# Kernel tuning notes

Measured on AMD Instinct MI355X. Metric: run time of the kernel, lower is better.

Reference implementation:

```python
import jax, jax.numpy as jnp
import numpy as np

HIDDEN_DIM = 256
CLIP_LEN = 2
B, NQ, T, D = 64, 10, 2048, 256


def setup_inputs() -> dict:
    key = jax.random.key(0)
    ks = jax.random.split(key, 10)
    s = 1.0 / np.sqrt(HIDDEN_DIM)  # torch GRU/Linear init scale
    return {
        "pred_logits": jax.random.normal(ks[0], (B, NQ, 2), jnp.float32),
        "pred_spans": jax.random.uniform(ks[1], (B, NQ, 2), jnp.float32),
        "memory": jax.random.normal(ks[2], (B, T, D), jnp.float32),
        "src_vid": jax.random.normal(ks[3], (B, T, D), jnp.float32),
        "W_ih": jax.random.normal(ks[4], (3 * D, D), jnp.float32) * s,
        "W_hh": jax.random.normal(ks[5], (3 * D, D), jnp.float32) * s,
        "b_ih": jax.random.normal(ks[6], (3 * D,), jnp.float32) * s,
        "b_hh": jax.random.normal(ks[7], (3 * D,), jnp.float32) * s,
        "W_sal": jax.random.normal(ks[8], (D, D), jnp.float32) * s,
        "b_sal": jax.random.normal(ks[9], (D,), jnp.float32) * s,
    }


def _gru_last_hidden(x, W_ih, W_hh, b_ih, b_hh):
    # x: [B, T, D] -> final hidden state [B, D] (torch nn.GRU, h0 = 0)
    b, t, d = x.shape
    gi = jnp.einsum("btd,gd->btg", x, W_ih) + b_ih  # [B, T, 3D], precompute input gates

    def step(h, gi_t):
        gh = jnp.einsum("bd,gd->bg", h, W_hh) + b_hh
        ir, iz, inn = jnp.split(gi_t, 3, axis=-1)
        hr, hz, hn = jnp.split(gh, 3, axis=-1)
        r = jax.nn.sigmoid(ir + hr)
        z = jax.nn.sigmoid(iz + hz)
        n = jnp.tanh(inn + r * hn)
        h_new = (1.0 - z) * n + z * h
        return h_new, None

    h0 = jnp.zeros((b, d), x.dtype)
    hT, _ = jax.lax.scan(step, h0, jnp.swapaxes(gi, 0, 1))
    return hT


def reference(pred_logits, pred_spans, memory, src_vid, W_ih, W_hh, b_ih, b_hh, W_sal, b_sal):
    b, t, d = memory.shape
    # top-1 span selection (sort descending, take first == argmax of class-0 prob)
    scores = jax.nn.softmax(pred_logits, axis=-1)[..., 0]  # [B, NQ]
    best = jnp.argmax(scores, axis=-1)  # [B]
    span = jnp.take_along_axis(pred_spans, best[:, None, None], axis=1)[:, 0, :]  # [B, 2] (cx, w)
    cx, w = span[:, 0], span[:, 1]
    xx = jnp.stack([cx - 0.5 * w, cx + 0.5 * w], axis=-1) * (t * CLIP_LEN)
    se = jnp.floor(xx / CLIP_LEN).astype(jnp.int32)  # [B, 2] start/end frame indices
    start = jnp.clip(se[:, 0], 0, t - 1)
    end_eff = jnp.minimum(se[:, 1], t - 1)
    # on-device dynamic slice + zero pad to fixed length T (replaces python loop)
    idx = start[:, None] + jnp.arange(t)[None, :]  # [B, T]
    valid = idx <= end_eff[:, None]  # empty slice if end < start
    idx_c = jnp.clip(idx, 0, t - 1)
    sliced = jnp.take_along_axis(src_vid, idx_c[..., None], axis=1) * valid[..., None].astype(src_vid.dtype)
    # GRU over padded slice, take last hidden
    hidden = _gru_last_hidden(sliced, W_ih, W_hh, b_ih, b_hh)  # [B, D]
    weight = jnp.einsum("bd,btd->bt", hidden, src_vid)  # [B, T]
    mem = memory * weight[..., None] + memory
    proj = jnp.einsum("btd,ed->bte", mem, W_sal) + b_sal
    saliency = jnp.sum(proj, axis=-1) / np.sqrt(HIDDEN_DIM)
    return saliency  # [B, T]
```

## Files before the change

kernel.cpp:

```cpp
#include <hip/hip_runtime.h>
#include <hip/hip_bf16.h>
#include <stdint.h>

#define T_SEQ 2048
#define DDIM 256
#define G3 768
#define NB 64
#define NQR 10

typedef _Float16 h2f __attribute__((ext_vector_type(2)));
typedef unsigned u32x4 __attribute__((ext_vector_type(4)));

__device__ __forceinline__ float fdot2u(unsigned a, unsigned b, float c) {
    return __builtin_amdgcn_fdot2(__builtin_bit_cast(h2f, a),
                                  __builtin_bit_cast(h2f, b), c, false);
}
__device__ __forceinline__ unsigned packf16(float a, float b) {
    auto p = __builtin_amdgcn_cvt_pkrtz(a, b);
    return __builtin_bit_cast(unsigned, p);
}
__device__ __forceinline__ float unpk(unsigned u, int hi) {
    unsigned w = hi ? (u >> 16) : u;
    h2f p = __builtin_bit_cast(h2f, w);
    return (float)p[0];
}
__device__ __forceinline__ float sigmf(float x) { return 1.0f / (1.0f + __expf(-x)); }
__device__ __forceinline__ float tanhff(float x) {
    float ax = fabsf(x);
    float e = __expf(2.0f * ax);
    float t = 1.0f - 2.0f / (e + 1.0f);
    return copysignf(t, x);
}

#define PIN4(x) asm volatile("" : "+v"(x))

__global__ __launch_bounds__(256) void k_prologue(
    const float* __restrict__ logits, const float* __restrict__ spans,
    const float* __restrict__ W_sal, const float* __restrict__ b_sal,
    int* __restrict__ meta, float* __restrict__ wcol, float* __restrict__ bsum) {
    int tid = threadIdx.x;
    if (tid < NB) {
        int b = tid;
        float bestv = -1e30f; int best = 0;
        for (int q = 0; q < NQR; ++q) {
            float l0 = logits[(b * NQR + q) * 2 + 0];
            float l1 = logits[(b * NQR + q) * 2 + 1];
            float sc = sigmf(l0 - l1);
            if (sc > bestv) { bestv = sc; best = q; }
        }
        float cx = spans[(b * NQR + best) * 2 + 0];
        float w  = spans[(b * NQR + best) * 2 + 1];
        float x0 = (cx - 0.5f * w) * (float)(T_SEQ * 2);
        float x1 = (cx + 0.5f * w) * (float)(T_SEQ * 2);
        int se0 = (int)floorf(x0 * 0.5f);
        int se1 = (int)floorf(x1 * 0.5f);
        int start = min(max(se0, 0), T_SEQ - 1);
        int end_eff = min(se1, T_SEQ - 1);
        int len = end_eff - start + 1;
        if (len < 0) len = 0;
        meta[b] = start; meta[NB + b] = len;
    }
    float acc = 0.f;
    for (int e = 0; e < DDIM; ++e) acc += W_sal[e * DDIM + tid];
    wcol[tid] = acc;
    if (tid < 64) {
        float p = b_sal[tid] + b_sal[tid + 64] + b_sal[tid + 128] + b_sal[tid + 192];
        for (int off = 32; off; off >>= 1) p += __shfl_down(p, off, 64);
        if (tid == 0) *bsum = p;
    }
}

__global__ __launch_bounds__(256) void k_prep(
    const float* __restrict__ W_ih, const float* __restrict__ W_hh,
    float* __restrict__ wt_ih, unsigned* __restrict__ w4) {
    int g = blockIdx.x, k = threadIdx.x;
    wt_ih[k * G3 + g] = W_ih[g * DDIM + k];
    if (k < 128) {
        unsigned v = packf16(W_hh[g * DDIM + 2 * k], W_hh[g * DDIM + 2 * k + 1]);
        w4[((k >> 2) * G3 + g) * 4 + (k & 3)] = v;
    }
}

__global__ __launch_bounds__(256) void k_gemm(
    const float* __restrict__ src_vid, const float* __restrict__ wt_ih,
    const float* __restrict__ b_ih, const int* __restrict__ meta,
    unsigned* __restrict__ gi2, int t0, int tc, int TC) {
    int b = blockIdx.y;
    int len = meta[NB + b];
    int tb = t0 + blockIdx.x * 16;
    int tcap = t0 + tc; if (tcap > len) tcap = len;
    if (tb >= tcap) return;
    int start = meta[b];
    int j = threadIdx.x;
    int nval = tcap - tb; if (nval > 16) nval = 16;
    float aR[16], aZ[16], aN[16];
    float bR = b_ih[j], bZ = b_ih[DDIM + j], bN = b_ih[2 * DDIM + j];
#pragma unroll
    for (int r = 0; r < 16; ++r) { aR[r] = bR; aZ[r] = bZ; aN[r] = bN; }
    const float* xb = src_vid + ((size_t)b * T_SEQ + start + tb) * DDIM;
    for (int kq = 0; kq < 64; ++kq) {
        float4 xq[16];
#pragma unroll
        for (int r = 0; r < 16; ++r) {
            if (r < nval) xq[r] = *(const float4*)(xb + r * DDIM + kq * 4);
            else          xq[r] = make_float4(0.f, 0.f, 0.f, 0.f);
        }
#pragma unroll
        for (int e = 0; e < 4; ++e) {
            int k = kq * 4 + e;
            float wR = wt_ih[k * G3 + j];
            float wZ = wt_ih[k * G3 + DDIM + j];
            float wN = wt_ih[k * G3 + 2 * DDIM + j];
#pragma unroll
            for (int r = 0; r < 16; ++r) {
                float xv = (e == 0) ? xq[r].x : (e == 1) ? xq[r].y : (e == 2) ? xq[r].z : xq[r].w;
                aR[r] = fmaf(xv, wR, aR[r]);
                aZ[r] = fmaf(xv, wZ, aZ[r]);
                aN[r] = fmaf(xv, wN, aN[r]);
            }
        }
    }
    unsigned* go = gi2 + ((size_t)b * TC + (tb - t0)) * 384;
    for (int r = 0; r < nval; ++r) {
        float oR = __shfl_xor(aR[r], 1, 64);
        float oZ = __shfl_xor(aZ[r], 1, 64);
        float oN = __shfl_xor(aN[r], 1, 64);
        if (!(j & 1)) {
            unsigned* gw = go + (size_t)r * 384 + (j >> 1);
            gw[0]   = packf16(aR[r], oR);
            gw[128] = packf16(aZ[r], oZ);
            gw[256] = packf16(aN[r], oN);
        }
    }
}

__global__ void __launch_bounds__(512)
__attribute__((amdgpu_waves_per_eu(2, 2))) k_gru(
    const unsigned* __restrict__ gi2, const unsigned* __restrict__ w4,
    const float* __restrict__ b_ih, const float* __restrict__ b_hh,
    const int* __restrict__ meta, float* __restrict__ h_state,
    int t0, int t1, int TC) {
    int b = blockIdx.x, tid = threadIdx.x;
    int c = tid & 255, half = tid >> 8;
    int len = meta[NB + b];

    u32x4 wrq[16], wzq[16], wnq[16];
    const u32x4* w4v = (const u32x4*)w4;
    const u32x4* wb = w4v + (size_t)(half * 16) * G3;
#pragma unroll
    for (int q = 0; q < 16; ++q) {
        wrq[q] = wb[q * G3 + c];
        wzq[q] = wb[q * G3 + 256 + c];
        wnq[q] = wb[q * G3 + 512 + c];
    }
#pragma unroll
    for (int q = 0; q < 16; ++q) { PIN4(wrq[q]); PIN4(wzq[q]); PIN4(wnq[q]); }

    float bhR = (half == 0) ? b_hh[c] : 0.f;
    float bhZ = (half == 0) ? b_hh[256 + c] : 0.f;
    float bhN = (half == 0) ? b_hh[512 + c] : 0.f;
    float biR = b_ih[c], biZ = b_ih[256 + c], biN = b_ih[512 + c];

    __shared__ unsigned hl[128];
    __shared__ float pl[3][256];

    float h = 0.f;
    if (half == 0) {
        if (t0 != 0) h = h_state[b * DDIM + c];
        float hp = __shfl_xor(h, 1, 64);
        if (!(c & 1)) hl[c >> 1] = packf16(h, hp);
    }

    const unsigned* gb2 = gi2 + (size_t)b * TC * 384 + (c >> 1);
    int sel = c & 1;
    float gR = biR, gZ = biZ, gN = biN;
    if (half == 0 && t0 < t1 && t0 < len) {
        gR = unpk(gb2[0], sel); gZ = unpk(gb2[128], sel); gN = unpk(gb2[256], sel);
    }
    __syncthreads();

    for (int t = t0; t < t1; ++t) {
        float nR = biR, nZ = biZ, nN = biN;
        int tn = t + 1;
        if (half == 0 && tn < t1 && tn < len) {
            const unsigned* gp = gb2 + (size_t)(tn - t0) * 384;
            nR = unpk(gp[0], sel); nZ = unpk(gp[128], sel); nN = unpk(gp[256], sel);
        }
#pragma unroll
        for (int q = 0; q < 16; ++q) { PIN4(wrq[q]); PIN4(wzq[q]); PIN4(wnq[q]); }
        float r0 = bhR, z0 = bhZ, n0 = bhN, r1 = 0.f, z1 = 0.f, n1 = 0.f;
        const u32x4* hb = (const u32x4*)hl + half * 16;
#pragma unroll
        for (int q = 0; q < 16; ++q) {
            u32x4 h4 = hb[q];
            r0 = fdot2u(h4.x, wrq[q].x, r0);
            z0 = fdot2u(h4.x, wzq[q].x, z0);
            n0 = fdot2u(h4.x, wnq[q].x, n0);
            r1 = fdot2u(h4.y, wrq[q].y, r1);
            z1 = fdot2u(h4.y, wzq[q].y, z1);
            n1 = fdot2u(h4.y, wnq[q].y, n1);
            r0 = fdot2u(h4.z, wrq[q].z, r0);
            z0 = fdot2u(h4.z, wzq[q].z, z0);
            n0 = fdot2u(h4.z, wnq[q].z, n0);
            r1 = fdot2u(h4.w, wrq[q].w, r1);
            z1 = fdot2u(h4.w, wzq[q].w, z1);
            n1 = fdot2u(h4.w, wnq[q].w, n1);
        }
        float hr = r0 + r1, hz = z0 + z1, hn = n0 + n1;
        if (half == 1) {
            pl[0][c] = hr; pl[1][c] = hz; pl[2][c] = hn;
        }
        __syncthreads();
        if (half == 0) {
            hr += pl[0][c]; hz += pl[1][c]; hn += pl[2][c];
            float r = sigmf(gR + hr);
            float z = sigmf(gZ + hz);
            float n = tanhff(gN + r * hn);
            h = (1.0f - z) * n + z * h;
            float hp = __shfl_xor(h, 1, 64);
            if (!(c & 1)) hl[c >> 1] = packf16(h, hp);
        }
        gR = nR; gZ = nZ; gN = nN;
        __syncthreads();
    }
    if (half == 0) h_state[b * DDIM + c] = h;
}

__global__ __launch_bounds__(256) void k_epi(
    const float* __restrict__ memory, const float* __restrict__ src_vid,
    const float* __restrict__ h_state, const float* __restrict__ wcol,
    const float* __restrict__ bsum, float* __restrict__ out) {
    int wid = blockIdx.x * 4 + (threadIdx.x >> 6);
    int lane = threadIdx.x & 63;
    int b = wid >> 11;
    int t = wid & 2047;
    const float4* mp = (const float4*)(memory + ((size_t)b * T_SEQ + t) * DDIM);
    const float4* sp = (const float4*)(src_vid + ((size_t)b * T_SEQ + t) * DDIM);
    const float4* hp = (const float4*)(h_state + b * DDIM);
    const float4* wp = (const float4*)wcol;
    float4 m = mp[lane], s = sp[lane], hv = hp[lane], wc = wp[lane];
    float s1 = m.x * wc.x + m.y * wc.y + m.z * wc.z + m.w * wc.w;
    float s2 = hv.x * s.x + hv.y * s.y + hv.z * s.z + hv.w * s.w;
    for (int off = 32; off; off >>= 1) {
        s1 += __shfl_down(s1, off, 64);
        s2 += __shfl_down(s2, off, 64);
    }
    if (lane == 0) out[(size_t)b * T_SEQ + t] = ((1.0f + s2) * s1 + *bsum) * 0.0625f;
}

extern "C" void kernel_launch(void* const* d_in, const int* in_sizes, int n_in,
                              void* d_out, int out_size, void* d_ws, size_t ws_size,
                              hipStream_t stream) {
    const float* logits  = (const float*)d_in[0];
    const float* spans   = (const float*)d_in[1];
    const float* memory  = (const float*)d_in[2];
    const float* src_vid = (const float*)d_in[3];
    const float* W_ih    = (const float*)d_in[4];
    const float* W_hh    = (const float*)d_in[5];
    const float* b_ih    = (const float*)d_in[6];
    const float* b_hh    = (const float*)d_in[7];
    const float* W_sal   = (const float*)d_in[8];
    const float* b_sal   = (const float*)d_in[9];
    float* out = (float*)d_out;
    char* ws = (char*)d_ws;

    const size_t OFF_META = 0;
    const size_t OFF_WCOL = 1024;
    const size_t OFF_BSUM = 2048;
    const size_t OFF_H    = 4096;
    const size_t OFF_W4   = 69632;
    const size_t OFF_WTIH = 462848;
    const size_t OFF_GI   = 1249280;

    int* meta       = (int*)(ws + OFF_META);
    float* wcol     = (float*)(ws + OFF_WCOL);
    float* bsum     = (float*)(ws + OFF_BSUM);
    float* h_state  = (float*)(ws + OFF_H);
    unsigned* w4    = (unsigned*)(ws + OFF_W4);
    float* wt_ih    = (float*)(ws + OFF_WTIH);
    unsigned* gi2   = (unsigned*)(ws + OFF_GI);

    size_t gi_cap = (ws_size > OFF_GI) ? (ws_size - OFF_GI) : 0;
    long long tc_max = (long long)(gi_cap / ((size_t)NB * 384 * 4));
    int TC = (tc_max > T_SEQ) ? T_SEQ : (int)tc_max;
    if (TC < 16) TC = 16;

    k_prologue<<<dim3(1), dim3(256), 0, stream>>>(logits, spans, W_sal, b_sal, meta, wcol, bsum);
    k_prep<<<dim3(G3), dim3(256), 0, stream>>>(W_ih, W_hh, wt_ih, w4);
    for (int t0 = 0; t0 < T_SEQ; t0 += TC) {
        int tc = T_SEQ - t0; if (tc > TC) tc = TC;
        k_gemm<<<dim3((tc + 15) / 16, NB), dim3(256), 0, stream>>>(
            src_vid, wt_ih, b_ih, meta, gi2, t0, tc, TC);
        k_gru<<<dim3(NB), dim3(512), 0, stream>>>(
            gi2, w4, b_ih, b_hh, meta, h_state, t0, t0 + tc, TC);
    }
    k_epi<<<dim3(NB * T_SEQ / 4), dim3(256), 0, stream>>>(
        memory, src_vid, h_state, wcol, bsum, out);
}
```

Before: 2.993 ms.

## Compute GRU r/z recurrent gates with MFMA waves, n gate on separate waves

Splits the per-batch GRU block into 8 waves that compute the r and z recurrent matvecs with 16x16x32 f16 MFMA, using W_hh fragments pre-swizzled by a new prep kernel, plus 4 waves that compute the n-gate dot products with fdot2 and run the gate update. The aim is to shorten the per-step latency of the serial recurrence by offloading two thirds of the recurrent work to matrix units and running it alongside the n-gate work. Each MFMA uses the broadcast hidden vector as the A operand, so only one of its 16 rows is used. The change also adds an extra weight layout in the workspace, which shrinks the gi chunk capacity, and keeps two barriers per step.

```diff
diff --git a/kernel.cpp b/kernel.cpp
--- a/kernel.cpp
+++ b/kernel.cpp
@@ -9,6 +9,8 @@
 #define NQR 10
 
 typedef _Float16 h2f __attribute__((ext_vector_type(2)));
+typedef _Float16 f16x8 __attribute__((ext_vector_type(8)));
+typedef float f32x4 __attribute__((ext_vector_type(4)));
 typedef unsigned u32x4 __attribute__((ext_vector_type(4)));
 
 __device__ __forceinline__ float fdot2u(unsigned a, unsigned b, float c) {
@@ -20,9 +22,8 @@
     return __builtin_bit_cast(unsigned, p);
 }
 __device__ __forceinline__ float unpk(unsigned u, int hi) {
-    unsigned w = hi ? (u >> 16) : u;
-    h2f p = __builtin_bit_cast(h2f, w);
-    return (float)p[0];
+    h2f p = __builtin_bit_cast(h2f, u);
+    return hi ? (float)p[1] : (float)p[0];
 }
 __device__ __forceinline__ float sigmf(float x) { return 1.0f / (1.0f + __expf(-x)); }
 __device__ __forceinline__ float tanhff(float x) {
@@ -31,8 +32,6 @@
     float t = 1.0f - 2.0f / (e + 1.0f);
     return copysignf(t, x);
 }
-
-#define PIN4(x) asm volatile("" : "+v"(x))
 
 __global__ __launch_bounds__(256) void k_prologue(
     const float* __restrict__ logits, const float* __restrict__ spans,
@@ -79,6 +78,18 @@
         unsigned v = packf16(W_hh[g * DDIM + 2 * k], W_hh[g * DDIM + 2 * k + 1]);
         w4[((k >> 2) * G3 + g) * 4 + (k & 3)] = v;
     }
+}
+
+__global__ __launch_bounds__(256) void k_prep2(
+    const float* __restrict__ W_hh, unsigned* __restrict__ wfrag) {
+    int u = blockIdx.x * 256 + threadIdx.x;
+    int jj = u & 3;
+    int l  = (u >> 2) & 63;
+    int kc = (u >> 8) & 7;
+    int wt = u >> 11;
+    int col = wt * 16 + (l & 15);
+    int k = kc * 32 + ((l >> 4) << 3) + jj * 2;
+    wfrag[u] = packf16(W_hh[col * DDIM + k], W_hh[col * DDIM + k + 1]);
 }
 
 __global__ __launch_bounds__(256) void k_gemm(
@@ -134,96 +145,112 @@
     }
 }
 
-__global__ void __launch_bounds__(512)
-__attribute__((amdgpu_waves_per_eu(2, 2))) k_gru(
+__global__ void __launch_bounds__(768) k_gru(
     const unsigned* __restrict__ gi2, const unsigned* __restrict__ w4,
+    const unsigned* __restrict__ wfrag,
     const float* __restrict__ b_ih, const float* __restrict__ b_hh,
     const int* __restrict__ meta, float* __restrict__ h_state,
     int t0, int t1, int TC) {
     int b = blockIdx.x, tid = threadIdx.x;
-    int c = tid & 255, half = tid >> 8;
+    int lane = tid & 63, w = tid >> 6;
     int len = meta[NB + b];
 
-    u32x4 wrq[16], wzq[16], wnq[16];
-    const u32x4* w4v = (const u32x4*)w4;
-    const u32x4* wb = w4v + (size_t)(half * 16) * G3;
-#pragma unroll
-    for (int q = 0; q < 16; ++q) {
-        wrq[q] = wb[q * G3 + c];
-        wzq[q] = wb[q * G3 + 256 + c];
-        wnq[q] = wb[q * G3 + 512 + c];
-    }
-#pragma unroll
-    for (int q = 0; q < 16; ++q) { PIN4(wrq[q]); PIN4(wzq[q]); PIN4(wnq[q]); }
-
-    float bhR = (half == 0) ? b_hh[c] : 0.f;
-    float bhZ = (half == 0) ? b_hh[256 + c] : 0.f;
-    float bhN = (half == 0) ? b_hh[512 + c] : 0.f;
-    float biR = b_ih[c], biZ = b_ih[256 + c], biN = b_ih[512 + c];
-
     __shared__ unsigned hl[128];
-    __shared__ float pl[3][256];
-
-    float h = 0.f;
-    if (half == 0) {
+    __shared__ float rz[512];
+
+    const f32x4 zf = {0.f, 0.f, 0.f, 0.f};
+
+    if (w < 8) {
+        int g = w >> 2;
+        int tq = w & 3;
+        u32x4 bf[32];
+        const u32x4* wfr = (const u32x4*)wfrag;
+#pragma unroll
+        for (int t4 = 0; t4 < 4; ++t4)
+#pragma unroll
+            for (int kc = 0; kc < 8; ++kc) {
+                int wt = g * 16 + tq * 4 + t4;
+                bf[t4 * 8 + kc] = wfr[(size_t)(wt * 8 + kc) * 64 + lane];
+            }
+        __syncthreads();
+        for (int t = t0; t < t1; ++t) {
+            f32x4 cf[4];
+            const u32x4* hb = (const u32x4*)hl;
+#pragma unroll
+            for (int kc = 0; kc < 8; ++kc) {
+                u32x4 av = hb[kc * 4 + (lane >> 4)];
+                f16x8 af = __builtin_bit_cast(f16x8, av);
+#pragma unroll
+                for (int t4 = 0; t4 < 4; ++t4) {
+                    cf[t4] = __builtin_amdgcn_mfma_f32_16x16x32_f16(
+                        af, __builtin_bit_cast(f16x8, bf[t4 * 8 + kc]),
+                        (kc == 0) ? zf : cf[t4], 0, 0, 0);
+                }
+            }
+            if (lane < 16) {
+#pragma unroll
+                for (int t4 = 0; t4 < 4; ++t4)
+                    rz[g * 256 + (tq * 4 + t4) * 16 + lane] = cf[t4][0];
+            }
+            __syncthreads();
+            __syncthreads();
+        }
+    } else {
+        int c = tid - 512;
+        u32x4 nq[32];
+        const u32x4* w4v = (const u32x4*)w4;
+#pragma unroll
+        for (int q = 0; q < 32; ++q) nq[q] = w4v[(size_t)q * G3 + 512 + c];
+
+        float bhR = b_hh[c], bhZ = b_hh[256 + c], bhN = b_hh[512 + c];
+        float biR = b_ih[c], biZ = b_ih[256 + c], biN = b_ih[512 + c];
+
+        float h = 0.f;
         if (t0 != 0) h = h_state[b * DDIM + c];
-        float hp = __shfl_xor(h, 1, 64);
-        if (!(c & 1)) hl[c >> 1] = packf16(h, hp);
-    }
-
-    const unsigned* gb2 = gi2 + (size_t)b * TC * 384 + (c >> 1);
-    int sel = c & 1;
-    float gR = biR, gZ = biZ, gN = biN;
-    if (half == 0 && t0 < t1 && t0 < len) {
-        gR = unpk(gb2[0], sel); gZ = unpk(gb2[128], sel); gN = unpk(gb2[256], sel);
-    }
-    __syncthreads();
-
-    for (int t = t0; t < t1; ++t) {
-        float nR = biR, nZ = biZ, nN = biN;
-        int tn = t + 1;
-        if (half == 0 && tn < t1 && tn < len) {
-            const unsigned* gp = gb2 + (size_t)(tn - t0) * 384;
-            nR = unpk(gp[0], sel); nZ = unpk(gp[128], sel); nN = unpk(gp[256], sel);
-        }
-#pragma unroll
-        for (int q = 0; q < 16; ++q) { PIN4(wrq[q]); PIN4(wzq[q]); PIN4(wnq[q]); }
-        float r0 = bhR, z0 = bhZ, n0 = bhN, r1 = 0.f, z1 = 0.f, n1 = 0.f;
-        const u32x4* hb = (const u32x4*)hl + half * 16;
-#pragma unroll
-        for (int q = 0; q < 16; ++q) {
-            u32x4 h4 = hb[q];
-            r0 = fdot2u(h4.x, wrq[q].x, r0);
-            z0 = fdot2u(h4.x, wzq[q].x, z0);
-            n0 = fdot2u(h4.x, wnq[q].x, n0);
-            r1 = fdot2u(h4.y, wrq[q].y, r1);
-            z1 = fdot2u(h4.y, wzq[q].y, z1);
-            n1 = fdot2u(h4.y, wnq[q].y, n1);
-            r0 = fdot2u(h4.z, wrq[q].z, r0);
-            z0 = fdot2u(h4.z, wzq[q].z, z0);
-            n0 = fdot2u(h4.z, wnq[q].z, n0);
-            r1 = fdot2u(h4.w, wrq[q].w, r1);
-            z1 = fdot2u(h4.w, wzq[q].w, z1);
-            n1 = fdot2u(h4.w, wnq[q].w, n1);
-        }
-        float hr = r0 + r1, hz = z0 + z1, hn = n0 + n1;
-        if (half == 1) {
-            pl[0][c] = hr; pl[1][c] = hz; pl[2][c] = hn;
+        {
+            float hp = __shfl_xor(h, 1, 64);
+            if (!(c & 1)) hl[c >> 1] = packf16(h, hp);
+        }
+        const unsigned* gb2 = gi2 + (size_t)b * TC * 384 + (c >> 1);
+        int sel = c & 1;
+        float gR = biR, gZ = biZ, gN = biN;
+        if (t0 < t1 && t0 < len) {
+            gR = unpk(gb2[0], sel); gZ = unpk(gb2[128], sel); gN = unpk(gb2[256], sel);
         }
         __syncthreads();
-        if (half == 0) {
-            hr += pl[0][c]; hz += pl[1][c]; hn += pl[2][c];
+
+        for (int t = t0; t < t1; ++t) {
+            float nR = biR, nZ = biZ, nN = biN;
+            int tn = t + 1;
+            if (tn < t1 && tn < len) {
+                const unsigned* gp = gb2 + (size_t)(tn - t0) * 384;
+                nR = unpk(gp[0], sel); nZ = unpk(gp[128], sel); nN = unpk(gp[256], sel);
+            }
+            float a0 = 0.f, a1 = 0.f, a2 = 0.f, a3 = 0.f;
+            const u32x4* hb = (const u32x4*)hl;
+#pragma unroll
+            for (int q = 0; q < 32; ++q) {
+                u32x4 h4 = hb[q];
+                a0 = fdot2u(h4.x, nq[q].x, a0);
+                a1 = fdot2u(h4.y, nq[q].y, a1);
+                a2 = fdot2u(h4.z, nq[q].z, a2);
+                a3 = fdot2u(h4.w, nq[q].w, a3);
+            }
+            float hn = bhN + (a0 + a1) + (a2 + a3);
+            __syncthreads();
+            float hr = rz[c] + bhR;
+            float hz = rz[256 + c] + bhZ;
             float r = sigmf(gR + hr);
             float z = sigmf(gZ + hz);
             float n = tanhff(gN + r * hn);
             h = (1.0f - z) * n + z * h;
             float hp = __shfl_xor(h, 1, 64);
             if (!(c & 1)) hl[c >> 1] = packf16(h, hp);
-        }
-        gR = nR; gZ = nZ; gN = nN;
-        __syncthreads();
-    }
-    if (half == 0) h_state[b * DDIM + c] = h;
+            gR = nR; gZ = nZ; gN = nN;
+            __syncthreads();
+        }
+        h_state[b * DDIM + c] = h;
+    }
 }
 
 __global__ __launch_bounds__(256) void k_epi(
@@ -269,14 +296,16 @@
     const size_t OFF_BSUM = 2048;
     const size_t OFF_H    = 4096;
     const size_t OFF_W4   = 69632;
-    const size_t OFF_WTIH = 462848;
-    const size_t OFF_GI   = 1249280;
+    const size_t OFF_FRAG = 462848;
+    const size_t OFF_WTIH = 856064;
+    const size_t OFF_GI   = 1642496;
 
     int* meta       = (int*)(ws + OFF_META);
     float* wcol     = (float*)(ws + OFF_WCOL);
     float* bsum     = (float*)(ws + OFF_BSUM);
     float* h_state  = (float*)(ws + OFF_H);
     unsigned* w4    = (unsigned*)(ws + OFF_W4);
+    unsigned* wfrag = (unsigned*)(ws + OFF_FRAG);
     float* wt_ih    = (float*)(ws + OFF_WTIH);
     unsigned* gi2   = (unsigned*)(ws + OFF_GI);
 
@@ -287,12 +316,13 @@
 
     k_prologue<<<dim3(1), dim3(256), 0, stream>>>(logits, spans, W_sal, b_sal, meta, wcol, bsum);
     k_prep<<<dim3(G3), dim3(256), 0, stream>>>(W_ih, W_hh, wt_ih, w4);
+    k_prep2<<<dim3(384), dim3(256), 0, stream>>>(W_hh, wfrag);
     for (int t0 = 0; t0 < T_SEQ; t0 += TC) {
         int tc = T_SEQ - t0; if (tc > TC) tc = TC;
         k_gemm<<<dim3((tc + 15) / 16, NB), dim3(256), 0, stream>>>(
             src_vid, wt_ih, b_ih, meta, gi2, t0, tc, TC);
-        k_gru<<<dim3(NB), dim3(512), 0, stream>>>(
-            gi2, w4, b_ih, b_hh, meta, h_state, t0, t0 + tc, TC);
+        k_gru<<<dim3(NB), dim3(768), 0, stream>>>(
+            gi2, w4, wfrag, b_ih, b_hh, meta, h_state, t0, t0 + tc, TC);
     }
     k_epi<<<dim3(NB * T_SEQ / 4), dim3(256), 0, stream>>>(
         memory, src_vid, h_state, wcol, bsum, out);
```

Measured after the change: 3.224 ms. 1.08x slower.

## Restructure GRU step to reduce K within wavefronts and double-buffer hidden state

Applied to the files above, without the earlier changes.

The recurrent GRU kernel is reorganized so each wavefront owns 32 output columns and splits the K dimension across four 16-lane groups, reducing partial sums with cross-lane shuffles instead of a shared-memory exchange between two thread halves. The hidden state is double-buffered in LDS, which removes one of the two block barriers per timestep. The LDS layout of h is permuted so each lane group reads its own K slice. This trades the second barrier and LDS round trip for extra shuffle instructions and drops the register-pinning asm and waves-per-eu hint, which may change register allocation.

```diff
diff --git a/kernel.cpp b/kernel.cpp
--- a/kernel.cpp
+++ b/kernel.cpp
@@ -20,9 +20,8 @@
     return __builtin_bit_cast(unsigned, p);
 }
 __device__ __forceinline__ float unpk(unsigned u, int hi) {
-    unsigned w = hi ? (u >> 16) : u;
-    h2f p = __builtin_bit_cast(h2f, w);
-    return (float)p[0];
+    h2f p = __builtin_bit_cast(h2f, u);
+    return hi ? (float)p[1] : (float)p[0];
 }
 __device__ __forceinline__ float sigmf(float x) { return 1.0f / (1.0f + __expf(-x)); }
 __device__ __forceinline__ float tanhff(float x) {
@@ -31,8 +30,6 @@
     float t = 1.0f - 2.0f / (e + 1.0f);
     return copysignf(t, x);
 }
-
-#define PIN4(x) asm volatile("" : "+v"(x))
 
 __global__ __launch_bounds__(256) void k_prologue(
     const float* __restrict__ logits, const float* __restrict__ spans,
@@ -134,96 +131,105 @@
     }
 }
 
-__global__ void __launch_bounds__(512)
-__attribute__((amdgpu_waves_per_eu(2, 2))) k_gru(
+__global__ void __launch_bounds__(512) k_gru(
     const unsigned* __restrict__ gi2, const unsigned* __restrict__ w4,
     const float* __restrict__ b_ih, const float* __restrict__ b_hh,
     const int* __restrict__ meta, float* __restrict__ h_state,
     int t0, int t1, int TC) {
     int b = blockIdx.x, tid = threadIdx.x;
-    int c = tid & 255, half = tid >> 8;
+    int lane = tid & 63, w = tid >> 6;
+    int kq = lane >> 4, lc = lane & 15;
+    int c0 = w * 32 + lc * 2;
     int len = meta[NB + b];
 
-    u32x4 wrq[16], wzq[16], wnq[16];
+    u32x4 wq[8][3][2];
     const u32x4* w4v = (const u32x4*)w4;
-    const u32x4* wb = w4v + (size_t)(half * 16) * G3;
-#pragma unroll
-    for (int q = 0; q < 16; ++q) {
-        wrq[q] = wb[q * G3 + c];
-        wzq[q] = wb[q * G3 + 256 + c];
-        wnq[q] = wb[q * G3 + 512 + c];
-    }
-#pragma unroll
-    for (int q = 0; q < 16; ++q) { PIN4(wrq[q]); PIN4(wzq[q]); PIN4(wnq[q]); }
-
-    float bhR = (half == 0) ? b_hh[c] : 0.f;
-    float bhZ = (half == 0) ? b_hh[256 + c] : 0.f;
-    float bhN = (half == 0) ? b_hh[512 + c] : 0.f;
-    float biR = b_ih[c], biZ = b_ih[256 + c], biN = b_ih[512 + c];
-
-    __shared__ unsigned hl[128];
-    __shared__ float pl[3][256];
+#pragma unroll
+    for (int q = 0; q < 8; ++q)
+#pragma unroll
+        for (int ga = 0; ga < 3; ++ga)
+#pragma unroll
+            for (int cc = 0; cc < 2; ++cc)
+                wq[q][ga][cc] = w4v[(size_t)(kq * 8 + q) * G3 + ga * 256 + c0 + cc];
+
+    int fc = c0 + (kq & 1);
+    float bhv[3], biv[3];
+#pragma unroll
+    for (int ga = 0; ga < 3; ++ga) {
+        bhv[ga] = b_hh[ga * 256 + fc];
+        biv[ga] = b_ih[ga * 256 + fc];
+    }
+
+    __shared__ unsigned hl[2][128];
 
     float h = 0.f;
-    if (half == 0) {
-        if (t0 != 0) h = h_state[b * DDIM + c];
-        float hp = __shfl_xor(h, 1, 64);
-        if (!(c & 1)) hl[c >> 1] = packf16(h, hp);
-    }
-
-    const unsigned* gb2 = gi2 + (size_t)b * TC * 384 + (c >> 1);
-    int sel = c & 1;
-    float gR = biR, gZ = biZ, gN = biN;
-    if (half == 0 && t0 < t1 && t0 < len) {
+    if (kq < 2 && t0 != 0) h = h_state[b * DDIM + fc];
+    {
+        float hx = __shfl_xor(h, 16, 64);
+        if (kq == 0) {
+            int p = c0 >> 1;
+            int loc = ((p >> 2) & 7) * 16 + ((p >> 5) << 2) + (p & 3);
+            hl[0][loc] = packf16(h, hx);
+        }
+    }
+
+    const unsigned* gb2 = gi2 + (size_t)b * TC * 384 + (fc >> 1);
+    int sel = fc & 1;
+    float gR = biv[0], gZ = biv[1], gN = biv[2];
+    if (kq < 2 && t0 < t1 && t0 < len) {
         gR = unpk(gb2[0], sel); gZ = unpk(gb2[128], sel); gN = unpk(gb2[256], sel);
     }
     __syncthreads();
 
+    int cur = 0;
     for (int t = t0; t < t1; ++t) {
-        float nR = biR, nZ = biZ, nN = biN;
+        float nR = biv[0], nZ = biv[1], nN = biv[2];
         int tn = t + 1;
-        if (half == 0 && tn < t1 && tn < len) {
+        if (kq < 2 && tn < t1 && tn < len) {
             const unsigned* gp = gb2 + (size_t)(tn - t0) * 384;
             nR = unpk(gp[0], sel); nZ = unpk(gp[128], sel); nN = unpk(gp[256], sel);
         }
-#pragma unroll
-        for (int q = 0; q < 16; ++q) { PIN4(wrq[q]); PIN4(wzq[q]); PIN4(wnq[q]); }
-        float r0 = bhR, z0 = bhZ, n0 = bhN, r1 = 0.f, z1 = 0.f, n1 = 0.f;
-        const u32x4* hb = (const u32x4*)hl + half * 16;
-#pragma unroll
-        for (int q = 0; q < 16; ++q) {
-            u32x4 h4 = hb[q];
-            r0 = fdot2u(h4.x, wrq[q].x, r0);
-            z0 = fdot2u(h4.x, wzq[q].x, z0);
-            n0 = fdot2u(h4.x, wnq[q].x, n0);
-            r1 = fdot2u(h4.y, wrq[q].y, r1);
-            z1 = fdot2u(h4.y, wzq[q].y, z1);
-            n1 = fdot2u(h4.y, wnq[q].y, n1);
-            r0 = fdot2u(h4.z, wrq[q].z, r0);
-            z0 = fdot2u(h4.z, wzq[q].z, z0);
-            n0 = fdot2u(h4.z, wnq[q].z, n0);
-            r1 = fdot2u(h4.w, wrq[q].w, r1);
-            z1 = fdot2u(h4.w, wzq[q].w, z1);
-            n1 = fdot2u(h4.w, wnq[q].w, n1);
-        }
-        float hr = r0 + r1, hz = z0 + z1, hn = n0 + n1;
-        if (half == 1) {
-            pl[0][c] = hr; pl[1][c] = hz; pl[2][c] = hn;
-        }
-        __syncthreads();
-        if (half == 0) {
-            hr += pl[0][c]; hz += pl[1][c]; hn += pl[2][c];
-            float r = sigmf(gR + hr);
-            float z = sigmf(gZ + hz);
-            float n = tanhff(gN + r * hn);
+        float ar0 = 0.f, az0 = 0.f, an0 = 0.f, ar1 = 0.f, az1 = 0.f, an1 = 0.f;
+        const u32x4* hb = (const u32x4*)hl[cur];
+#pragma unroll
+        for (int q = 0; q < 8; ++q) {
+            u32x4 hq = hb[q * 4 + kq];
+#pragma unroll
+            for (int e = 0; e < 4; ++e) {
+                ar0 = fdot2u(hq[e], wq[q][0][0][e], ar0);
+                az0 = fdot2u(hq[e], wq[q][1][0][e], az0);
+                an0 = fdot2u(hq[e], wq[q][2][0][e], an0);
+                ar1 = fdot2u(hq[e], wq[q][0][1][e], ar1);
+                az1 = fdot2u(hq[e], wq[q][1][1][e], az1);
+                an1 = fdot2u(hq[e], wq[q][2][1][e], an1);
+            }
+        }
+        ar0 += __shfl_xor(ar0, 16, 64); ar0 += __shfl_xor(ar0, 32, 64);
+        az0 += __shfl_xor(az0, 16, 64); az0 += __shfl_xor(az0, 32, 64);
+        an0 += __shfl_xor(an0, 16, 64); an0 += __shfl_xor(an0, 32, 64);
+        ar1 += __shfl_xor(ar1, 16, 64); ar1 += __shfl_xor(ar1, 32, 64);
+        az1 += __shfl_xor(az1, 16, 64); az1 += __shfl_xor(az1, 32, 64);
+        an1 += __shfl_xor(an1, 16, 64); an1 += __shfl_xor(an1, 32, 64);
+        if (kq < 2) {
+            float rs = (kq == 0) ? ar0 : ar1;
+            float zs = (kq == 0) ? az0 : az1;
+            float ns = (kq == 0) ? an0 : an1;
+            float r = sigmf(gR + rs + bhv[0]);
+            float z = sigmf(gZ + zs + bhv[1]);
+            float n = tanhff(gN + r * (ns + bhv[2]));
             h = (1.0f - z) * n + z * h;
-            float hp = __shfl_xor(h, 1, 64);
-            if (!(c & 1)) hl[c >> 1] = packf16(h, hp);
+        }
+        float hx = __shfl_xor(h, 16, 64);
+        if (kq == 0) {
+            int p = c0 >> 1;
+            int loc = ((p >> 2) & 7) * 16 + ((p >> 5) << 2) + (p & 3);
+            hl[cur ^ 1][loc] = packf16(h, hx);
         }
         gR = nR; gZ = nZ; gN = nN;
         __syncthreads();
-    }
-    if (half == 0) h_state[b * DDIM + c] = h;
+        cur ^= 1;
+    }
+    if (kq < 2) h_state[b * DDIM + fc] = h;
 }
 
 __global__ __launch_bounds__(256) void k_epi(
```

New measurement: 3.773 ms. 26.1% more time.

## Compute GRU input-gate projection with fp16 MFMA using pre-swizzled weight fragments

Applied to the files above, without the earlier changes.

Replaces the scalar-FMA input-gate GEMM with a matrix-core kernel: W_ih is pre-packed into fp16 MFMA B-fragments held in registers. Each block stages 16 timesteps of src_vid as fp16 in XOR-swizzled shared memory and runs 16x16x32 MFMAs. It also drops the register-pinning asm barriers and the waves_per_eu attribute in the GRU kernel, using launch_bounds(512,2) instead. Inputs are now rounded to fp16 before the projection, which adds some precision loss.

```diff
diff --git a/kernel.cpp b/kernel.cpp
--- a/kernel.cpp
+++ b/kernel.cpp
@@ -9,6 +9,8 @@
 #define NQR 10
 
 typedef _Float16 h2f __attribute__((ext_vector_type(2)));
+typedef _Float16 f16x8 __attribute__((ext_vector_type(8)));
+typedef float f32x4 __attribute__((ext_vector_type(4)));
 typedef unsigned u32x4 __attribute__((ext_vector_type(4)));
 
 __device__ __forceinline__ float fdot2u(unsigned a, unsigned b, float c) {
@@ -20,9 +22,8 @@
     return __builtin_bit_cast(unsigned, p);
 }
 __device__ __forceinline__ float unpk(unsigned u, int hi) {
-    unsigned w = hi ? (u >> 16) : u;
-    h2f p = __builtin_bit_cast(h2f, w);
-    return (float)p[0];
+    h2f p = __builtin_bit_cast(h2f, u);
+    return hi ? (float)p[1] : (float)p[0];
 }
 __device__ __forceinline__ float sigmf(float x) { return 1.0f / (1.0f + __expf(-x)); }
 __device__ __forceinline__ float tanhff(float x) {
@@ -31,8 +32,6 @@
     float t = 1.0f - 2.0f / (e + 1.0f);
     return copysignf(t, x);
 }
-
-#define PIN4(x) asm volatile("" : "+v"(x))
 
 __global__ __launch_bounds__(256) void k_prologue(
     const float* __restrict__ logits, const float* __restrict__ spans,
@@ -71,71 +70,102 @@
 }
 
 __global__ __launch_bounds__(256) void k_prep(
-    const float* __restrict__ W_ih, const float* __restrict__ W_hh,
-    float* __restrict__ wt_ih, unsigned* __restrict__ w4) {
+    const float* __restrict__ W_hh, unsigned* __restrict__ w4) {
     int g = blockIdx.x, k = threadIdx.x;
-    wt_ih[k * G3 + g] = W_ih[g * DDIM + k];
     if (k < 128) {
         unsigned v = packf16(W_hh[g * DDIM + 2 * k], W_hh[g * DDIM + 2 * k + 1]);
         w4[((k >> 2) * G3 + g) * 4 + (k & 3)] = v;
     }
 }
 
-__global__ __launch_bounds__(256) void k_gemm(
-    const float* __restrict__ src_vid, const float* __restrict__ wt_ih,
+__global__ __launch_bounds__(256) void k_prepI(
+    const float* __restrict__ W_ih, unsigned* __restrict__ wfragI) {
+    int u = blockIdx.x * 256 + threadIdx.x;
+    int jj = u & 3;
+    int l  = (u >> 2) & 63;
+    int kc = (u >> 8) & 7;
+    int ct = u >> 11;
+    int col = ct * 16 + (l & 15);
+    int k = kc * 32 + ((l >> 4) << 3) + jj * 2;
+    wfragI[u] = packf16(W_ih[col * DDIM + k], W_ih[col * DDIM + k + 1]);
+}
+
+__global__ __launch_bounds__(512, 2) void k_gemm(
+    const float* __restrict__ src_vid, const unsigned* __restrict__ wfragI,
     const float* __restrict__ b_ih, const int* __restrict__ meta,
     unsigned* __restrict__ gi2, int t0, int tc, int TC) {
     int b = blockIdx.y;
     int len = meta[NB + b];
-    int tb = t0 + blockIdx.x * 16;
-    int tcap = t0 + tc; if (tcap > len) tcap = len;
-    if (tb >= tcap) return;
     int start = meta[b];
-    int j = threadIdx.x;
-    int nval = tcap - tb; if (nval > 16) nval = 16;
-    float aR[16], aZ[16], aN[16];
-    float bR = b_ih[j], bZ = b_ih[DDIM + j], bN = b_ih[2 * DDIM + j];
-#pragma unroll
-    for (int r = 0; r < 16; ++r) { aR[r] = bR; aZ[r] = bZ; aN[r] = bN; }
-    const float* xb = src_vid + ((size_t)b * T_SEQ + start + tb) * DDIM;
-    for (int kq = 0; kq < 64; ++kq) {
-        float4 xq[16];
-#pragma unroll
-        for (int r = 0; r < 16; ++r) {
-            if (r < nval) xq[r] = *(const float4*)(xb + r * DDIM + kq * 4);
-            else          xq[r] = make_float4(0.f, 0.f, 0.f, 0.f);
-        }
-#pragma unroll
-        for (int e = 0; e < 4; ++e) {
-            int k = kq * 4 + e;
-            float wR = wt_ih[k * G3 + j];
-            float wZ = wt_ih[k * G3 + DDIM + j];
-            float wN = wt_ih[k * G3 + 2 * DDIM + j];
-#pragma unroll
-            for (int r = 0; r < 16; ++r) {
-                float xv = (e == 0) ? xq[r].x : (e == 1) ? xq[r].y : (e == 2) ? xq[r].z : xq[r].w;
-                aR[r] = fmaf(xv, wR, aR[r]);
-                aZ[r] = fmaf(xv, wZ, aZ[r]);
-                aN[r] = fmaf(xv, wN, aN[r]);
+    int tbase = t0 + blockIdx.x * 256;
+    int tend = t0 + tc; if (tend > len) tend = len;
+    int tcap = tbase + 256; if (tend > tcap) tend = tcap;
+    if (tbase >= tend) return;
+
+    int tid = threadIdx.x, lane = tid & 63, w = tid >> 6;
+
+    u32x4 bfr[6][8];
+    const u32x4* wf = (const u32x4*)wfragI;
+#pragma unroll
+    for (int j = 0; j < 6; ++j)
+#pragma unroll
+        for (int kc = 0; kc < 8; ++kc)
+            bfr[j][kc] = wf[((w * 6 + j) * 8 + kc) * 64 + lane];
+
+    int row = lane & 15, kg = lane >> 4;
+    float bv[6];
+#pragma unroll
+    for (int j = 0; j < 6; ++j) bv[j] = b_ih[(w * 6 + j) * 16 + row];
+
+    __shared__ unsigned As[2048];
+    int sr = tid >> 5, sx = tid & 31;
+
+    for (int tch = tbase; tch < tend; tch += 16) {
+        int tr = tch + sr;
+        u32x4 pk = {0u, 0u, 0u, 0u};
+        if (tr < len) {
+            const float* sp = src_vid + ((size_t)b * T_SEQ + start + tr) * DDIM + sx * 8;
+            float4 a0 = *(const float4*)sp;
+            float4 a1 = *(const float4*)(sp + 4);
+            pk[0] = packf16(a0.x, a0.y); pk[1] = packf16(a0.z, a0.w);
+            pk[2] = packf16(a1.x, a1.y); pk[3] = packf16(a1.z, a1.w);
+        }
+        *(u32x4*)&As[sr * 128 + ((sx ^ sr) << 2)] = pk;
+        __syncthreads();
+
+        f32x4 d[6];
+#pragma unroll
+        for (int j = 0; j < 6; ++j) d[j] = (f32x4){bv[j], bv[j], bv[j], bv[j]};
+#pragma unroll
+        for (int kc = 0; kc < 8; ++kc) {
+            u32x4 av = *(const u32x4*)&As[row * 128 + (((kc * 4 + kg) ^ row) << 2)];
+            f16x8 af = __builtin_bit_cast(f16x8, av);
+#pragma unroll
+            for (int j = 0; j < 6; ++j)
+                d[j] = __builtin_amdgcn_mfma_f32_16x16x32_f16(
+                    af, __builtin_bit_cast(f16x8, bfr[j][kc]), d[j], 0, 0, 0);
+        }
+
+#pragma unroll
+        for (int j = 0; j < 6; ++j) {
+            int cflat = (w * 6 + j) * 16 + row;
+            int gate = cflat >> 8;
+            int pairi = (cflat & 255) >> 1;
+#pragma unroll
+            for (int reg = 0; reg < 4; ++reg) {
+                int t = tch + kg * 4 + reg;
+                float v = d[j][reg];
+                float o = __shfl_xor(v, 1, 64);
+                if (!(lane & 1) && t < tend)
+                    gi2[((size_t)b * TC + (t - t0)) * 384 + gate * 128 + pairi] =
+                        packf16(v, o);
             }
         }
-    }
-    unsigned* go = gi2 + ((size_t)b * TC + (tb - t0)) * 384;
-    for (int r = 0; r < nval; ++r) {
-        float oR = __shfl_xor(aR[r], 1, 64);
-        float oZ = __shfl_xor(aZ[r], 1, 64);
-        float oN = __shfl_xor(aN[r], 1, 64);
-        if (!(j & 1)) {
-            unsigned* gw = go + (size_t)r * 384 + (j >> 1);
-            gw[0]   = packf16(aR[r], oR);
-            gw[128] = packf16(aZ[r], oZ);
-            gw[256] = packf16(aN[r], oN);
-        }
-    }
-}
-
-__global__ void __launch_bounds__(512)
-__attribute__((amdgpu_waves_per_eu(2, 2))) k_gru(
+        __syncthreads();
+    }
+}
+
+__global__ void __launch_bounds__(512, 2) k_gru(
     const unsigned* __restrict__ gi2, const unsigned* __restrict__ w4,
     const float* __restrict__ b_ih, const float* __restrict__ b_hh,
     const int* __restrict__ meta, float* __restrict__ h_state,
@@ -153,8 +183,6 @@
         wzq[q] = wb[q * G3 + 256 + c];
         wnq[q] = wb[q * G3 + 512 + c];
     }
-#pragma unroll
-    for (int q = 0; q < 16; ++q) { PIN4(wrq[q]); PIN4(wzq[q]); PIN4(wnq[q]); }
 
     float bhR = (half == 0) ? b_hh[c] : 0.f;
     float bhZ = (half == 0) ? b_hh[256 + c] : 0.f;
@@ -186,8 +214,6 @@
             const unsigned* gp = gb2 + (size_t)(tn - t0) * 384;
             nR = unpk(gp[0], sel); nZ = unpk(gp[128], sel); nN = unpk(gp[256], sel);
         }
-#pragma unroll
-        for (int q = 0; q < 16; ++q) { PIN4(wrq[q]); PIN4(wzq[q]); PIN4(wnq[q]); }
         float r0 = bhR, z0 = bhZ, n0 = bhN, r1 = 0.f, z1 = 0.f, n1 = 0.f;
         const u32x4* hb = (const u32x4*)hl + half * 16;
 #pragma unroll
@@ -269,15 +295,15 @@
     const size_t OFF_BSUM = 2048;
     const size_t OFF_H    = 4096;
     const size_t OFF_W4   = 69632;
-    const size_t OFF_WTIH = 462848;
-    const size_t OFF_GI   = 1249280;
+    const size_t OFF_WFI  = 462848;
+    const size_t OFF_GI   = 856064;
 
     int* meta       = (int*)(ws + OFF_META);
     float* wcol     = (float*)(ws + OFF_WCOL);
     float* bsum     = (float*)(ws + OFF_BSUM);
     float* h_state  = (float*)(ws + OFF_H);
     unsigned* w4    = (unsigned*)(ws + OFF_W4);
-    float* wt_ih    = (float*)(ws + OFF_WTIH);
+    unsigned* wfragI= (unsigned*)(ws + OFF_WFI);
     unsigned* gi2   = (unsigned*)(ws + OFF_GI);
 
     size_t gi_cap = (ws_size > OFF_GI) ? (ws_size - OFF_GI) : 0;
@@ -286,11 +312,12 @@
     if (TC < 16) TC = 16;
 
     k_prologue<<<dim3(1), dim3(256), 0, stream>>>(logits, spans, W_sal, b_sal, meta, wcol, bsum);
-    k_prep<<<dim3(G3), dim3(256), 0, stream>>>(W_ih, W_hh, wt_ih, w4);
+    k_prep<<<dim3(G3), dim3(256), 0, stream>>>(W_hh, w4);
+    k_prepI<<<dim3(384), dim3(256), 0, stream>>>(W_ih, wfragI);
     for (int t0 = 0; t0 < T_SEQ; t0 += TC) {
         int tc = T_SEQ - t0; if (tc > TC) tc = TC;
-        k_gemm<<<dim3((tc + 15) / 16, NB), dim3(256), 0, stream>>>(
-            src_vid, wt_ih, b_ih, meta, gi2, t0, tc, TC);
+        k_gemm<<<dim3((tc + 255) / 256, NB), dim3(512), 0, stream>>>(
+            src_vid, wfragI, b_ih, meta, gi2, t0, tc, TC);
         k_gru<<<dim3(NB), dim3(512), 0, stream>>>(
             gi2, w4, b_ih, b_hh, meta, h_state, t0, t0 + tc, TC);
     }
```

Result: faster. 2.572 ms (-14.1%).
